# Optimization experiments

Hardware: AMD Instinct MI355X
Metric: run time of the kernel (lower is better)

## Reference

```python
import jax, jax.numpy as jnp
import numpy as np

B, L, D, H, S = 2, 2048, 1024, 16, 4
Dh = D // H
EPS = 1e-5


def setup_inputs() -> dict:
    key = jax.random.key(0)
    ks = jax.random.split(key, 12)
    sc = 0.02
    w = lambda k, shape: (jax.random.normal(k, shape, jnp.float32) * sc)
    M = 2 * S  # number of MHA blocks / dense linears
    inp = {
        "response": jax.random.normal(ks[0], (B, L, D), jnp.float32),
        "mask": jnp.broadcast_to(jnp.tril(jnp.ones((L, L), bool)), (B, L, L)),
        "Wq": w(ks[1], (M, D, D)), "bq": w(ks[2], (M, D)),
        "Wk": w(ks[3], (M, D, D)), "bk": w(ks[4], (M, D)),
        "Wv": w(ks[5], (M, D, D)), "bv": w(ks[6], (M, D)),
        "Wo": w(ks[7], (M, D, D)), "bo": w(ks[8], (M, D)),
        "Wd": w(ks[9], (M, D, D)), "bd": w(ks[10], (M, D)),
    }
    return inp


def _ln(x):
    # fresh LayerNorm(d) with default weight=1, bias=0, eps=1e-5
    m = jnp.mean(x, axis=-1, keepdims=True)
    v = jnp.mean((x - m) ** 2, axis=-1, keepdims=True)
    return (x - m) * jax.lax.rsqrt(v + EPS)


def _linear(x, W, b):
    # torch Linear: x @ W.T + b
    return jnp.einsum('bld,od->blo', x, W) + b


def _mha(x, i, mask, Wq, bq, Wk, bk, Wv, bv, Wo, bo):
    # self-attention: q = k = v = x
    split = lambda y: y.reshape(B, L, H, Dh).transpose(0, 2, 1, 3)  # (B,H,L,Dh)
    q = split(_linear(x, Wq[i], bq[i]))
    k = split(_linear(x, Wk[i], bk[i]))
    v = split(_linear(x, Wv[i], bv[i]))
    scores = jnp.einsum('bhqd,bhkd->bhqk', q, k) / jnp.sqrt(jnp.float32(Dh))
    if mask is not None:
        scores = jnp.where(mask[:, None, :, :], scores, -jnp.inf)
    p = jnp.nan_to_num(jax.nn.softmax(scores, axis=-1))
    o = jnp.einsum('bhqk,bhkd->bhqd', p, v).transpose(0, 2, 1, 3).reshape(B, L, D)
    return _linear(o, Wo[i], bo[i])


def reference(response, mask, Wq, bq, Wk, bk, Wv, bv, Wo, bo, Wd, bd):
    x = response
    for i in range(S):
        # masked self-attention + residual + LN
        x = _ln(x + _mha(x, 2 * i, mask, Wq, bq, Wk, bk, Wv, bv, Wo, bo))
        # encoder-attention sublayer (encMem is None -> unmasked self-attention)
        x = _ln(x + _mha(x, 2 * i + 1, None, Wq, bq, Wk, bk, Wv, bv, Wo, bo))
        # dense: linear[2i](LeakyReLU(linear[2i+1](x)))
        h = jax.nn.leaky_relu(_linear(x, Wd[2 * i + 1], bd[2 * i + 1]), negative_slope=0.01)
        h = _linear(h, Wd[2 * i], bd[2 * i])
        x = _ln(x + h)
    return x
```

## Files before the change

kernel.cpp:

```cpp
#include <hip/hip_runtime.h>
#include <stdint.h>
#include <stddef.h>

typedef __attribute__((ext_vector_type(8))) _Float16 f16x8;
typedef __attribute__((ext_vector_type(4))) _Float16 f16x4;
typedef __attribute__((ext_vector_type(4))) float    f32x4;

#define NB 2
#define NL 2048
#define ND 1024
#define NH 16
#define NROWS (NB*NL)

__device__ __forceinline__ void async16(void* lds, const void* g) {
  __builtin_amdgcn_global_load_lds(
      (const __attribute__((address_space(1))) void*)g,
      (__attribute__((address_space(3))) void*)lds, 16, 0, 0);
}

struct CvtArgs { const float* in[5]; _Float16* out[5]; };

__global__ __launch_bounds__(256) void cvt_all(CvtArgs a, int n4)
{
  const float* in  = a.in[blockIdx.z];
  _Float16*   out  = a.out[blockIdx.z];
  for (int i = blockIdx.x * blockDim.x + threadIdx.x; i < n4;
       i += gridDim.x * blockDim.x) {
    float4 v = ((const float4*)in)[i];
    f16x4 o = {(_Float16)v.x, (_Float16)v.y, (_Float16)v.z, (_Float16)v.w};
    ((f16x4*)out)[i] = o;
  }
}

__global__ __launch_bounds__(256) void init_x(
    const float* __restrict__ r, float* __restrict__ x,
    _Float16* __restrict__ xh, int n4)
{
  for (int i = blockIdx.x * blockDim.x + threadIdx.x; i < n4;
       i += gridDim.x * blockDim.x) {
    float4 v = ((const float4*)r)[i];
    ((float4*)x)[i] = v;
    f16x4 o = {(_Float16)v.x, (_Float16)v.y, (_Float16)v.z, (_Float16)v.w};
    ((f16x4*)xh)[i] = o;
  }
}

struct GArgs {
  const _Float16* A;
  const _Float16* B[3];
  const float*    bias[3];
  void*           out[3];
  int             mode[3];
  int             ksplit;
};

__global__ __launch_bounds__(256, 2) void gemm_bt(GArgs ga)
{
  __shared__ _Float16 As[2][128 * 64];
  __shared__ _Float16 Bs[2][128 * 64];
  const int tid = threadIdx.x;
  const int w = tid >> 6, l = tid & 63;
  const int ql = l & 15, g = l >> 4;
  const int z = blockIdx.z;
  const int widx = ga.ksplit ? 0 : (blockIdx.x >> 3);
  const _Float16* Bw  = ga.B[widx];
  const float*   bias = ga.bias[widx];
  void*          outp = ga.ksplit ? ga.out[z] : ga.out[widx];
  const int      mode = ga.mode[widx];
  const int kbeg = ga.ksplit ? z * (ND / 2) : 0;
  const int kend = ga.ksplit ? kbeg + ND / 2 : ND;
  const bool dobias = (!ga.ksplit) || (z == 0);
  const int brow = blockIdx.y * 128;
  const int bcol = (blockIdx.x & 7) * 128;
  const int wm = w >> 1, wn = w & 1;
  f32x4 acc[4][4] = {};

  const int srow = w * 32 + (l >> 3);
  const int scol = ((l & 7) ^ (l >> 3)) << 3;
  const _Float16* Ag = ga.A + (size_t)(brow + srow) * ND + scol;
  const _Float16* Bg = Bw   + (size_t)(bcol + srow) * ND + scol;

#define STAGE(buf, k0_)                                                  \
  {                                                                      \
    _Float16* AsW = &As[buf][w * 2048];                                  \
    _Float16* BsW = &Bs[buf][w * 2048];                                  \
    _Pragma("unroll")                                                    \
    for (int i = 0; i < 4; ++i) {                                        \
      async16(AsW + i * 512, Ag + (size_t)i * 8 * ND + (k0_));           \
      async16(BsW + i * 512, Bg + (size_t)i * 8 * ND + (k0_));           \
    }                                                                    \
  }

  STAGE(0, kbeg);
  for (int k0 = kbeg; k0 < kend; k0 += 64) {
    const int cur = ((k0 - kbeg) >> 6) & 1;
    if (k0 + 64 < kend) {
      STAGE(cur ^ 1, k0 + 64);
      asm volatile("s_waitcnt vmcnt(8)" ::: "memory");
    } else {
      asm volatile("s_waitcnt vmcnt(0)" ::: "memory");
    }
    __builtin_amdgcn_s_barrier();
#pragma unroll
    for (int ks = 0; ks < 64; ks += 32) {
      const int cx = (ks + g * 8) ^ ((ql & 7) << 3);
      f16x8 af[4], bf[4];
#pragma unroll
      for (int mi = 0; mi < 4; ++mi)
        af[mi] = *(const f16x8*)&As[cur][(wm * 64 + mi * 16 + ql) * 64 + cx];
#pragma unroll
      for (int nj = 0; nj < 4; ++nj)
        bf[nj] = *(const f16x8*)&Bs[cur][(wn * 64 + nj * 16 + ql) * 64 + cx];
#pragma unroll
      for (int mi = 0; mi < 4; ++mi)
#pragma unroll
        for (int nj = 0; nj < 4; ++nj)
          acc[mi][nj] = __builtin_amdgcn_mfma_f32_16x16x32_f16(
              af[mi], bf[nj], acc[mi][nj], 0, 0, 0);
    }
    asm volatile("s_waitcnt lgkmcnt(0)" ::: "memory");
    __builtin_amdgcn_s_barrier();
  }
#undef STAGE

  const int colb = bcol + wn * 64;
  const int rowb = brow + wm * 64 + g * 4;
  if (mode == 3) {
    _Float16* vt = (_Float16*)outp;
    const int bb = rowb >> 11;
#pragma unroll
    for (int nj = 0; nj < 4; ++nj) {
      const int col = colb + nj * 16 + ql;
      const float bv = bias[col];
      const int hh = col >> 6, d = col & 63;
      _Float16* vrow = vt + ((size_t)((bb * NH + hh) * 64 + d)) * NL;
#pragma unroll
      for (int mi = 0; mi < 4; ++mi) {
        const int krow = (rowb + mi * 16) & (NL - 1);
        f16x4 o;
#pragma unroll
        for (int r = 0; r < 4; ++r) o[r] = (_Float16)(acc[mi][nj][r] + bv);
        *(f16x4*)(vrow + krow) = o;
      }
    }
  } else {
    _Float16* oh = (_Float16*)outp;
#pragma unroll
    for (int nj = 0; nj < 4; ++nj) {
      const int col = colb + nj * 16 + ql;
      const float bv = dobias ? bias[col] : 0.f;
#pragma unroll
      for (int mi = 0; mi < 4; ++mi) {
#pragma unroll
        for (int r = 0; r < 4; ++r) {
          float v = acc[mi][nj][r] + bv;
          if (mode == 2) v = v > 0.f ? v : 0.01f * v;
          oh[(size_t)(rowb + mi * 16 + r) * ND + col] = (_Float16)v;
        }
      }
    }
  }
}

template<bool CAUSAL>
__global__ __launch_bounds__(256, 3) void attn_fwd(
    const _Float16* __restrict__ Q, const _Float16* __restrict__ K,
    const _Float16* __restrict__ Vt, _Float16* __restrict__ O)
{
  __shared__ _Float16 kv[2][2][64 * 64];
  __shared__ unsigned int pls[4][2][16 * 34];
  const int tid = threadIdx.x;
  const int w = tid >> 6, l = tid & 63;
  const int ql = l & 15, g = l >> 4;
  const int h = blockIdx.y, b = blockIdx.z;
  const int qt = (CAUSAL && b) ? (NL / 128 - 1 - (int)blockIdx.x) : blockIdx.x;

  f16x8 bq[2][2];
  int qrow[2];
#pragma unroll
  for (int f = 0; f < 2; ++f) {
    qrow[f] = qt * 128 + w * 32 + f * 16 + ql;
    const _Float16* Qp = Q + (size_t)(b * NL + qrow[f]) * ND + h * 64 + g * 8;
    bq[f][0] = *(const f16x8*)Qp;
    bq[f][1] = *(const f16x8*)(Qp + 32);
  }

  const int srow = w * 16 + (l >> 3);
  const int scol = ((l & 7) ^ (l >> 3)) << 3;
  const _Float16* Kg = K  + ((size_t)(b * NL) + srow) * ND + h * 64 + scol;
  const _Float16* Vg = Vt + ((size_t)((b * NH + h) * 64 + srow)) * NL + scol;

  const int msk  = (ql & 7) << 3;
  const int offA = ql * 64 + ((     g * 8) ^ msk);
  const int offB = ql * 64 + ((32 + g * 8) ^ msk);

  f32x4 ot[2][4] = {};
  float s_run[2] = {0.f, 0.f};
  const int ntiles = CAUSAL ? (qt * 2 + 2) : (NL / 64);
  const float SCL = 0.125f * 1.44269504089f;
  const float M2  = 4.0f * 1.44269504089f;

  async16(&kv[0][0][w * 1024      ], Kg);
  async16(&kv[0][0][w * 1024 + 512], Kg + (size_t)8 * ND);
  async16(&kv[0][1][w * 1024      ], Vg);
  async16(&kv[0][1][w * 1024 + 512], Vg + (size_t)8 * NL);

  for (int kt = 0; kt < ntiles; ++kt) {
    const int nb = kt & 1;
    const size_t nk0 = (size_t)((kt + 1 < ntiles) ? kt + 1 : kt) * 64;
    async16(&kv[nb ^ 1][0][w * 1024      ], Kg + nk0 * ND);
    async16(&kv[nb ^ 1][0][w * 1024 + 512], Kg + nk0 * ND + (size_t)8 * ND);
    async16(&kv[nb ^ 1][1][w * 1024      ], Vg + nk0);
    async16(&kv[nb ^ 1][1][w * 1024 + 512], Vg + nk0 + (size_t)8 * NL);
    asm volatile("s_waitcnt vmcnt(4)" ::: "memory");
    __builtin_amdgcn_s_barrier();

    const _Float16* kb = &kv[nb][0][0];
    const _Float16* vb = &kv[nb][1][0];
    const int k0 = kt * 64;

#pragma unroll
    for (int f = 0; f < 2; ++f) {
      f32x4 st[4] = {};
#pragma unroll
      for (int sub = 0; sub < 4; ++sub) {
        const f16x8 a0 = *(const f16x8*)&kb[sub * 1024 + offA];
        const f16x8 a1 = *(const f16x8*)&kb[sub * 1024 + offB];
        st[sub] = __builtin_amdgcn_mfma_f32_16x16x32_f16(a0, bq[f][0], st[sub], 0, 0, 0);
        st[sub] = __builtin_amdgcn_mfma_f32_16x16x32_f16(a1, bq[f][1], st[sub], 0, 0, 0);
      }
      float ps = 0.f;
      float pv[16];
#pragma unroll
      for (int sub = 0; sub < 4; ++sub)
#pragma unroll
        for (int r = 0; r < 4; ++r) {
          float p = exp2f(__builtin_fmaf(st[sub][r], SCL, -M2));
          if (CAUSAL && (k0 + sub * 16 + g * 4 + r) > qrow[f]) p = 0.f;
          pv[sub * 4 + r] = p;
          ps += p;
        }
#pragma unroll
      for (int sub = 0; sub < 4; ++sub) {
        uint2 uu;
        uu.x = __builtin_bit_cast(unsigned int,
                  __builtin_amdgcn_cvt_pkrtz(pv[sub * 4 + 0], pv[sub * 4 + 1]));
        uu.y = __builtin_bit_cast(unsigned int,
                  __builtin_amdgcn_cvt_pkrtz(pv[sub * 4 + 2], pv[sub * 4 + 3]));
        *(uint2*)&pls[w][f][(sub * 4 + g) * 34 + 2 * ql] = uu;
      }
      ps += __shfl_xor(ps, 16);
      ps += __shfl_xor(ps, 32);
      s_run[f] += ps;
    }

#pragma unroll
    for (int hh = 0; hh < 2; ++hh) {
      f16x8 pf[2];
#pragma unroll
      for (int f = 0; f < 2; ++f) {
        uint2 lo = *(const uint2*)&pls[w][f][(hh * 8 + 2 * g    ) * 34 + 2 * ql];
        uint2 hi = *(const uint2*)&pls[w][f][(hh * 8 + 2 * g + 1) * 34 + 2 * ql];
        uint4 ui; ui.x = lo.x; ui.y = lo.y; ui.z = hi.x; ui.w = hi.y;
        pf[f] = __builtin_bit_cast(f16x8, ui);
      }
      const int voff = hh ? offB : offA;
#pragma unroll
      for (int dt = 0; dt < 4; ++dt) {
        const f16x8 vf = *(const f16x8*)&vb[dt * 1024 + voff];
        ot[0][dt] = __builtin_amdgcn_mfma_f32_16x16x32_f16(vf, pf[0], ot[0][dt], 0, 0, 0);
        ot[1][dt] = __builtin_amdgcn_mfma_f32_16x16x32_f16(vf, pf[1], ot[1][dt], 0, 0, 0);
      }
    }
    asm volatile("s_waitcnt lgkmcnt(0)" ::: "memory");
    __builtin_amdgcn_s_barrier();
  }

#pragma unroll
  for (int f = 0; f < 2; ++f) {
    const float inv = 1.f / s_run[f];
#pragma unroll
    for (int dt = 0; dt < 4; ++dt) {
      f16x4 o;
#pragma unroll
      for (int r = 0; r < 4; ++r) o[r] = (_Float16)(ot[f][dt][r] * inv);
      *(f16x4*)(O + (size_t)(b * NL + qrow[f]) * ND + h * 64 + dt * 16 + g * 4) = o;
    }
  }
}

__global__ __launch_bounds__(256) void resid_ln(
    const float* __restrict__ x, const _Float16* __restrict__ d0,
    const _Float16* __restrict__ d1,
    float* __restrict__ xo, _Float16* __restrict__ xh)
{
  const int row = blockIdx.x, tid = threadIdx.x;
  const float4 xv = ((const float4*)(x + (size_t)row * ND))[tid];
  const f16x4 v0 = ((const f16x4*)(d0 + (size_t)row * ND))[tid];
  const f16x4 v1 = ((const f16x4*)(d1 + (size_t)row * ND))[tid];
  const float a = xv.x + (float)v0[0] + (float)v1[0];
  const float b = xv.y + (float)v0[1] + (float)v1[1];
  const float c = xv.z + (float)v0[2] + (float)v1[2];
  const float d = xv.w + (float)v0[3] + (float)v1[3];
  float s = a + b + c + d;
  float ss = a * a + b * b + c * c + d * d;
#pragma unroll
  for (int m = 1; m < 64; m <<= 1) {
    s  += __shfl_xor(s, m);
    ss += __shfl_xor(ss, m);
  }
  __shared__ float red[8];
  if ((tid & 63) == 0) { red[tid >> 6] = s; red[4 + (tid >> 6)] = ss; }
  __syncthreads();
  const float S  = red[0] + red[1] + red[2] + red[3];
  const float SS = red[4] + red[5] + red[6] + red[7];
  const float mean = S * (1.0f / ND);
  const float var  = SS * (1.0f / ND) - mean * mean;
  const float rstd = rsqrtf(fmaxf(var, 0.f) + 1e-5f);
  float4 y;
  y.x = (a - mean) * rstd; y.y = (b - mean) * rstd;
  y.z = (c - mean) * rstd; y.w = (d - mean) * rstd;
  ((float4*)(xo + (size_t)row * ND))[tid] = y;
  f16x4 yh = {(_Float16)y.x, (_Float16)y.y, (_Float16)y.z, (_Float16)y.w};
  ((f16x4*)(xh + (size_t)row * ND))[tid] = yh;
}

extern "C" void kernel_launch(void* const* d_in, const int* in_sizes, int n_in,
                              void* d_out, int out_size, void* d_ws, size_t ws_size,
                              hipStream_t stream)
{
  (void)in_sizes; (void)n_in; (void)out_size; (void)ws_size;
  const float* response = (const float*)d_in[0];
  const float* Wq = (const float*)d_in[2];
  const float* bq = (const float*)d_in[3];
  const float* Wk = (const float*)d_in[4];
  const float* bk = (const float*)d_in[5];
  const float* Wv = (const float*)d_in[6];
  const float* bv = (const float*)d_in[7];
  const float* Wo = (const float*)d_in[8];
  const float* bo = (const float*)d_in[9];
  const float* Wd = (const float*)d_in[10];
  const float* bd = (const float*)d_in[11];
  float* x = (float*)d_out;

  const size_t MB = 1024 * 1024;
  char* p = (char*)d_ws;
  _Float16* Wq_h = (_Float16*)(p + 0 * MB);
  _Float16* Wk_h = (_Float16*)(p + 16 * MB);
  _Float16* Wv_h = (_Float16*)(p + 32 * MB);
  _Float16* Wo_h = (_Float16*)(p + 48 * MB);
  _Float16* Wd_h = (_Float16*)(p + 64 * MB);
  _Float16* xh   = (_Float16*)(p + 80 * MB);
  _Float16* Qh   = (_Float16*)(p + 88 * MB);
  _Float16* Kh   = (_Float16*)(p + 96 * MB);
  _Float16* Vth  = (_Float16*)(p + 104 * MB);
  _Float16* Oh   = (_Float16*)(p + 112 * MB);
  _Float16* h1   = Qh;
  _Float16* t0   = (_Float16*)(p + 96 * MB);
  _Float16* t1   = (_Float16*)(p + 104 * MB);

  const int wn4 = 8 * 1024 * 1024 / 4;
  CvtArgs ca = { { Wq, Wk, Wv, Wo, Wd }, { Wq_h, Wk_h, Wv_h, Wo_h, Wd_h } };
  cvt_all<<<dim3(256, 1, 5), 256, 0, stream>>>(ca, wn4);
  init_x<<<1024, 256, 0, stream>>>(response, x, xh, NROWS * ND / 4);

  const dim3 g3(24, NROWS / 128, 1);
  const dim3 gs(8, NROWS / 128, 2);
  const dim3 gf(8, NROWS / 128, 1);
  const dim3 agrid(NL / 128, NH, NB);

  for (int i = 0; i < 4; ++i) {
    for (int sub = 0; sub < 2; ++sub) {
      const int m = 2 * i + sub;
      const size_t wo = (size_t)m * MB;
      const size_t bf = (size_t)m * 1024;
      GArgs qkv = { xh,
                    { Wq_h + wo, Wk_h + wo, Wv_h + wo },
                    { bq + bf, bk + bf, bv + bf },
                    { Qh, Kh, Vth }, { 0, 0, 3 }, 0 };
      gemm_bt<<<g3, 256, 0, stream>>>(qkv);
      if (sub == 0) attn_fwd<true ><<<agrid, 256, 0, stream>>>(Qh, Kh, Vth, Oh);
      else          attn_fwd<false><<<agrid, 256, 0, stream>>>(Qh, Kh, Vth, Oh);
      GArgs oprj = { Oh,
                     { Wo_h + wo, nullptr, nullptr },
                     { bo + bf, nullptr, nullptr },
                     { t0, t1, nullptr }, { 0, 0, 0 }, 1 };
      gemm_bt<<<gs, 256, 0, stream>>>(oprj);
      resid_ln<<<NROWS, 256, 0, stream>>>(x, t0, t1, x, xh);
    }
    const size_t w1 = (size_t)(2 * i + 1) * MB, b1 = (size_t)(2 * i + 1) * 1024;
    const size_t w0 = (size_t)(2 * i) * MB,     b0 = (size_t)(2 * i) * 1024;
    GArgs f1 = { xh,
                 { Wd_h + w1, nullptr, nullptr },
                 { bd + b1, nullptr, nullptr },
                 { h1, nullptr, nullptr }, { 2, 0, 0 }, 0 };
    gemm_bt<<<gf, 256, 0, stream>>>(f1);
    GArgs f2 = { h1,
                 { Wd_h + w0, nullptr, nullptr },
                 { bd + b0, nullptr, nullptr },
                 { t0, t1, nullptr }, { 0, 0, 0 }, 1 };
    gemm_bt<<<gs, 256, 0, stream>>>(f2);
    resid_ln<<<NROWS, 256, 0, stream>>>(x, t0, t1, x, xh);
  }
}
```

Measured before the change: 1.354 ms.

## Split attention across 8 waves with triple-buffered K/V and one barrier

The attention kernel now runs 512 threads with 8 waves, each handling 16 query rows instead of 32, so there are more waves per block for latency hiding. K/V staging becomes a three-buffer ring, and each wave loads half as much per tile. This lets the trailing end-of-iteration barrier and its lgkmcnt wait be dropped, leaving one barrier per tile. The P staging buffer per wave shrinks and is reused for each half of the PV product. In exchange, each K/V fragment read from LDS feeds only one query fragment, so LDS read traffic per FLOP roughly doubles. The wave count per CU is also bounded by the larger LDS footprint.

```diff
diff --git a/kernel.cpp b/kernel.cpp
--- a/kernel.cpp
+++ b/kernel.cpp
@@ -163,29 +163,24 @@
 }
 
 template<bool CAUSAL>
-__global__ __launch_bounds__(256, 3) void attn_fwd(
+__global__ __launch_bounds__(512, 4) void attn_fwd(
     const _Float16* __restrict__ Q, const _Float16* __restrict__ K,
     const _Float16* __restrict__ Vt, _Float16* __restrict__ O)
 {
-  __shared__ _Float16 kv[2][2][64 * 64];
-  __shared__ unsigned int pls[4][2][16 * 34];
+  __shared__ _Float16 kv[3][2][64 * 64];
+  __shared__ unsigned int pls[8][8 * 34];
   const int tid = threadIdx.x;
   const int w = tid >> 6, l = tid & 63;
   const int ql = l & 15, g = l >> 4;
   const int h = blockIdx.y, b = blockIdx.z;
   const int qt = (CAUSAL && b) ? (NL / 128 - 1 - (int)blockIdx.x) : blockIdx.x;
-
-  f16x8 bq[2][2];
-  int qrow[2];
-#pragma unroll
-  for (int f = 0; f < 2; ++f) {
-    qrow[f] = qt * 128 + w * 32 + f * 16 + ql;
-    const _Float16* Qp = Q + (size_t)(b * NL + qrow[f]) * ND + h * 64 + g * 8;
-    bq[f][0] = *(const f16x8*)Qp;
-    bq[f][1] = *(const f16x8*)(Qp + 32);
-  }
-
-  const int srow = w * 16 + (l >> 3);
+  const int qrow = qt * 128 + w * 16 + ql;
+
+  const _Float16* Qp = Q + (size_t)(b * NL + qrow) * ND + h * 64 + g * 8;
+  const f16x8 bq0 = *(const f16x8*)Qp;
+  const f16x8 bq1 = *(const f16x8*)(Qp + 32);
+
+  const int srow = w * 8 + (l >> 3);
   const int scol = ((l & 7) ^ (l >> 3)) << 3;
   const _Float16* Kg = K  + ((size_t)(b * NL) + srow) * ND + h * 64 + scol;
   const _Float16* Vg = Vt + ((size_t)((b * NH + h) * 64 + srow)) * NL + scol;
@@ -194,98 +189,101 @@
   const int offA = ql * 64 + ((     g * 8) ^ msk);
   const int offB = ql * 64 + ((32 + g * 8) ^ msk);
 
-  f32x4 ot[2][4] = {};
-  float s_run[2] = {0.f, 0.f};
+  unsigned int* pw = &pls[w][0];
+  f32x4 ot[4] = {};
+  float s_run = 0.f;
   const int ntiles = CAUSAL ? (qt * 2 + 2) : (NL / 64);
   const float SCL = 0.125f * 1.44269504089f;
   const float M2  = 4.0f * 1.44269504089f;
 
-  async16(&kv[0][0][w * 1024      ], Kg);
-  async16(&kv[0][0][w * 1024 + 512], Kg + (size_t)8 * ND);
-  async16(&kv[0][1][w * 1024      ], Vg);
-  async16(&kv[0][1][w * 1024 + 512], Vg + (size_t)8 * NL);
-
+  async16(&kv[0][0][w * 512], Kg);
+  async16(&kv[0][1][w * 512], Vg);
+
+  int cbuf = 0, sbuf = 1;
   for (int kt = 0; kt < ntiles; ++kt) {
-    const int nb = kt & 1;
     const size_t nk0 = (size_t)((kt + 1 < ntiles) ? kt + 1 : kt) * 64;
-    async16(&kv[nb ^ 1][0][w * 1024      ], Kg + nk0 * ND);
-    async16(&kv[nb ^ 1][0][w * 1024 + 512], Kg + nk0 * ND + (size_t)8 * ND);
-    async16(&kv[nb ^ 1][1][w * 1024      ], Vg + nk0);
-    async16(&kv[nb ^ 1][1][w * 1024 + 512], Vg + nk0 + (size_t)8 * NL);
-    asm volatile("s_waitcnt vmcnt(4)" ::: "memory");
+    async16(&kv[sbuf][0][w * 512], Kg + nk0 * ND);
+    async16(&kv[sbuf][1][w * 512], Vg + nk0);
+    asm volatile("s_waitcnt vmcnt(2)" ::: "memory");
     __builtin_amdgcn_s_barrier();
 
-    const _Float16* kb = &kv[nb][0][0];
-    const _Float16* vb = &kv[nb][1][0];
+    const _Float16* kb = &kv[cbuf][0][0];
+    const _Float16* vb = &kv[cbuf][1][0];
     const int k0 = kt * 64;
-
-#pragma unroll
-    for (int f = 0; f < 2; ++f) {
-      f32x4 st[4] = {};
-#pragma unroll
-      for (int sub = 0; sub < 4; ++sub) {
-        const f16x8 a0 = *(const f16x8*)&kb[sub * 1024 + offA];
-        const f16x8 a1 = *(const f16x8*)&kb[sub * 1024 + offB];
-        st[sub] = __builtin_amdgcn_mfma_f32_16x16x32_f16(a0, bq[f][0], st[sub], 0, 0, 0);
-        st[sub] = __builtin_amdgcn_mfma_f32_16x16x32_f16(a1, bq[f][1], st[sub], 0, 0, 0);
+    f32x4 st[4] = {};
+#pragma unroll
+    for (int sub = 0; sub < 4; ++sub) {
+      const f16x8 a0 = *(const f16x8*)&kb[sub * 1024 + offA];
+      const f16x8 a1 = *(const f16x8*)&kb[sub * 1024 + offB];
+      st[sub] = __builtin_amdgcn_mfma_f32_16x16x32_f16(a0, bq0, st[sub], 0, 0, 0);
+      st[sub] = __builtin_amdgcn_mfma_f32_16x16x32_f16(a1, bq1, st[sub], 0, 0, 0);
+    }
+    float ps = 0.f;
+    float pv[16];
+#pragma unroll
+    for (int sub = 0; sub < 4; ++sub)
+#pragma unroll
+      for (int r = 0; r < 4; ++r) {
+        float p = exp2f(__builtin_fmaf(st[sub][r], SCL, -M2));
+        if (CAUSAL && (k0 + sub * 16 + g * 4 + r) > qrow) p = 0.f;
+        pv[sub * 4 + r] = p;
+        ps += p;
       }
-      float ps = 0.f;
-      float pv[16];
-#pragma unroll
-      for (int sub = 0; sub < 4; ++sub)
-#pragma unroll
-        for (int r = 0; r < 4; ++r) {
-          float p = exp2f(__builtin_fmaf(st[sub][r], SCL, -M2));
-          if (CAUSAL && (k0 + sub * 16 + g * 4 + r) > qrow[f]) p = 0.f;
-          pv[sub * 4 + r] = p;
-          ps += p;
-        }
-#pragma unroll
-      for (int sub = 0; sub < 4; ++sub) {
-        uint2 uu;
-        uu.x = __builtin_bit_cast(unsigned int,
-                  __builtin_amdgcn_cvt_pkrtz(pv[sub * 4 + 0], pv[sub * 4 + 1]));
-        uu.y = __builtin_bit_cast(unsigned int,
-                  __builtin_amdgcn_cvt_pkrtz(pv[sub * 4 + 2], pv[sub * 4 + 3]));
-        *(uint2*)&pls[w][f][(sub * 4 + g) * 34 + 2 * ql] = uu;
+    ps += __shfl_xor(ps, 16);
+    ps += __shfl_xor(ps, 32);
+    s_run += ps;
+
+#pragma unroll
+    for (int sub = 0; sub < 2; ++sub) {
+      uint2 uu;
+      uu.x = __builtin_bit_cast(unsigned int,
+                __builtin_amdgcn_cvt_pkrtz(pv[sub * 4 + 0], pv[sub * 4 + 1]));
+      uu.y = __builtin_bit_cast(unsigned int,
+                __builtin_amdgcn_cvt_pkrtz(pv[sub * 4 + 2], pv[sub * 4 + 3]));
+      *(uint2*)&pw[(sub * 4 + g) * 34 + 2 * ql] = uu;
+    }
+    {
+      uint2 lo = *(const uint2*)&pw[(2 * g    ) * 34 + 2 * ql];
+      uint2 hi = *(const uint2*)&pw[(2 * g + 1) * 34 + 2 * ql];
+      uint4 ui; ui.x = lo.x; ui.y = lo.y; ui.z = hi.x; ui.w = hi.y;
+      const f16x8 pf = __builtin_bit_cast(f16x8, ui);
+#pragma unroll
+      for (int dt = 0; dt < 4; ++dt) {
+        const f16x8 vf = *(const f16x8*)&vb[dt * 1024 + offA];
+        ot[dt] = __builtin_amdgcn_mfma_f32_16x16x32_f16(vf, pf, ot[dt], 0, 0, 0);
       }
-      ps += __shfl_xor(ps, 16);
-      ps += __shfl_xor(ps, 32);
-      s_run[f] += ps;
-    }
-
-#pragma unroll
-    for (int hh = 0; hh < 2; ++hh) {
-      f16x8 pf[2];
-#pragma unroll
-      for (int f = 0; f < 2; ++f) {
-        uint2 lo = *(const uint2*)&pls[w][f][(hh * 8 + 2 * g    ) * 34 + 2 * ql];
-        uint2 hi = *(const uint2*)&pls[w][f][(hh * 8 + 2 * g + 1) * 34 + 2 * ql];
-        uint4 ui; ui.x = lo.x; ui.y = lo.y; ui.z = hi.x; ui.w = hi.y;
-        pf[f] = __builtin_bit_cast(f16x8, ui);
+    }
+#pragma unroll
+    for (int sub = 2; sub < 4; ++sub) {
+      uint2 uu;
+      uu.x = __builtin_bit_cast(unsigned int,
+                __builtin_amdgcn_cvt_pkrtz(pv[sub * 4 + 0], pv[sub * 4 + 1]));
+      uu.y = __builtin_bit_cast(unsigned int,
+                __builtin_amdgcn_cvt_pkrtz(pv[sub * 4 + 2], pv[sub * 4 + 3]));
+      *(uint2*)&pw[((sub - 2) * 4 + g) * 34 + 2 * ql] = uu;
+    }
+    {
+      uint2 lo = *(const uint2*)&pw[(2 * g    ) * 34 + 2 * ql];
+      uint2 hi = *(const uint2*)&pw[(2 * g + 1) * 34 + 2 * ql];
+      uint4 ui; ui.x = lo.x; ui.y = lo.y; ui.z = hi.x; ui.w = hi.y;
+      const f16x8 pf = __builtin_bit_cast(f16x8, ui);
+#pragma unroll
+      for (int dt = 0; dt < 4; ++dt) {
+        const f16x8 vf = *(const f16x8*)&vb[dt * 1024 + offB];
+        ot[dt] = __builtin_amdgcn_mfma_f32_16x16x32_f16(vf, pf, ot[dt], 0, 0, 0);
       }
-      const int voff = hh ? offB : offA;
-#pragma unroll
-      for (int dt = 0; dt < 4; ++dt) {
-        const f16x8 vf = *(const f16x8*)&vb[dt * 1024 + voff];
-        ot[0][dt] = __builtin_amdgcn_mfma_f32_16x16x32_f16(vf, pf[0], ot[0][dt], 0, 0, 0);
-        ot[1][dt] = __builtin_amdgcn_mfma_f32_16x16x32_f16(vf, pf[1], ot[1][dt], 0, 0, 0);
-      }
-    }
-    asm volatile("s_waitcnt lgkmcnt(0)" ::: "memory");
-    __builtin_amdgcn_s_barrier();
-  }
-
-#pragma unroll
-  for (int f = 0; f < 2; ++f) {
-    const float inv = 1.f / s_run[f];
-#pragma unroll
-    for (int dt = 0; dt < 4; ++dt) {
-      f16x4 o;
-#pragma unroll
-      for (int r = 0; r < 4; ++r) o[r] = (_Float16)(ot[f][dt][r] * inv);
-      *(f16x4*)(O + (size_t)(b * NL + qrow[f]) * ND + h * 64 + dt * 16 + g * 4) = o;
-    }
+    }
+    cbuf = sbuf;
+    sbuf = sbuf + 1 == 3 ? 0 : sbuf + 1;
+  }
+
+  const float inv = 1.f / s_run;
+#pragma unroll
+  for (int dt = 0; dt < 4; ++dt) {
+    f16x4 o;
+#pragma unroll
+    for (int r = 0; r < 4; ++r) o[r] = (_Float16)(ot[dt][r] * inv);
+    *(f16x4*)(O + (size_t)(b * NL + qrow) * ND + h * 64 + dt * 16 + g * 4) = o;
   }
 }
 
@@ -379,8 +377,8 @@
                     { bq + bf, bk + bf, bv + bf },
                     { Qh, Kh, Vth }, { 0, 0, 3 }, 0 };
       gemm_bt<<<g3, 256, 0, stream>>>(qkv);
-      if (sub == 0) attn_fwd<true ><<<agrid, 256, 0, stream>>>(Qh, Kh, Vth, Oh);
-      else          attn_fwd<false><<<agrid, 256, 0, stream>>>(Qh, Kh, Vth, Oh);
+      if (sub == 0) attn_fwd<true ><<<agrid, 512, 0, stream>>>(Qh, Kh, Vth, Oh);
+      else          attn_fwd<false><<<agrid, 512, 0, stream>>>(Qh, Kh, Vth, Oh);
       GArgs oprj = { Oh,
                      { Wo_h + wo, nullptr, nullptr },
                      { bo + bf, nullptr, nullptr },
```

Result: faster. 1.237 ms (-8.6%).
